# Performance work log

Hardware: AMD Instinct MI355X
Metric: run time of the kernel (lower is better)

Reference implementation:

```python
import jax, jax.numpy as jnp
import numpy as np

B, S, D = 2, 2048, 1024
H, HD = 16, 64  # num heads, head dim
EPS = 1e-12
SCALING = HD ** -0.5


def rotate_half(x):
    x1, x2 = jnp.split(x, 2, axis=-1)
    return jnp.concatenate([-x2, x1], axis=-1)


def setup_inputs() -> dict:
    key = jax.random.key(0)
    ks = jax.random.split(key, 12)
    hidden_states = jax.random.normal(ks[0], (B, S, D), dtype=jnp.float32)
    # RoPE tables (standard rotate-half convention)
    inv_freq = 1.0 / (10000.0 ** (np.arange(0, HD, 2, dtype=np.float32) / HD))
    pos = np.arange(S, dtype=np.float32)
    freqs = np.outer(pos, inv_freq)  # [S, HD/2]
    emb = np.concatenate([freqs, freqs], axis=-1)  # [S, HD]
    cos = jnp.asarray(np.cos(emb))
    sin = jnp.asarray(np.sin(emb))
    w = 0.02
    return {
        "hidden_states": hidden_states,
        "cos": cos,
        "sin": sin,
        "Wq": jax.random.normal(ks[1], (D, D), dtype=jnp.float32) * w,
        "bq": jnp.zeros((D,), dtype=jnp.float32),
        "Wk": jax.random.normal(ks[2], (D, D), dtype=jnp.float32) * w,
        "bk": jnp.zeros((D,), dtype=jnp.float32),
        "Wv": jax.random.normal(ks[3], (D, D), dtype=jnp.float32) * w,
        "bv": jnp.zeros((D,), dtype=jnp.float32),
        "Wo": jax.random.normal(ks[4], (D, D), dtype=jnp.float32) * w,
        "bo": jnp.zeros((D,), dtype=jnp.float32),
        "ln_w": jnp.ones((D,), dtype=jnp.float32),
        "ln_b": jnp.zeros((D,), dtype=jnp.float32),
    }


def reference(hidden_states, cos, sin, Wq, bq, Wk, bk, Wv, bv, Wo, bo, ln_w, ln_b):
    b, s, d = hidden_states.shape
    # QKV projections -> [b, h, s, hd]
    def proj(W, bias):
        return (hidden_states @ W.T + bias).reshape(b, s, H, HD).transpose(0, 2, 1, 3)
    q, k, v = proj(Wq, bq), proj(Wk, bk), proj(Wv, bv)
    # RoPE (cos/sin broadcast over batch and head dims)
    c = cos[None, None, :, :]
    sn = sin[None, None, :, :]
    q = q * c + rotate_half(q) * sn
    k = k * c + rotate_half(k) * sn
    # Faithful to source: query pre-scaled AND scaling applied inside attention
    q = q * SCALING
    scores = jnp.einsum("bhsd,bhtd->bhst", q, k) * SCALING
    attn = jax.nn.softmax(scores, axis=-1)
    ctx = jnp.einsum("bhst,bhtd->bhsd", attn, v)  # [b,h,s,hd]
    ctx = ctx.transpose(0, 2, 1, 3).reshape(b, s, d)
    # output dense + residual + LayerNorm
    out = ctx @ Wo.T + bo + hidden_states
    mu = jnp.mean(out, axis=-1, keepdims=True)
    var = jnp.var(out, axis=-1, keepdims=True)
    return (out - mu) / jnp.sqrt(var + EPS) * ln_w + ln_b
```

## Files before the change

### kernel.cpp

```cpp
#include <hip/hip_runtime.h>
#include <hip/hip_bf16.h>
#include <stdint.h>


typedef unsigned short ushort_t;
typedef short bf16x8 __attribute__((ext_vector_type(8)));
typedef float f32x4 __attribute__((ext_vector_type(4)));
typedef float f32x16 __attribute__((ext_vector_type(16)));
typedef unsigned short ushort8 __attribute__((ext_vector_type(8)));

#define LOG2E 1.4426950408889634f

__device__ __forceinline__ ushort_t f2b(float f) {
  uint32_t x = __builtin_bit_cast(uint32_t, f);
  return (ushort_t)((x + 0x7FFFu + ((x >> 16) & 1u)) >> 16);
}

__device__ __forceinline__ uint32_t cvt_pk_bf16(float lo, float hi) {
  uint32_t r;
  asm("v_cvt_pk_bf16_f32 %0, %1, %2" : "=v"(r) : "v"(lo), "v"(hi));
  return r;
}

__device__ __forceinline__ void permswap(uint32_t& a, uint32_t& b) {
  asm volatile("v_permlane32_swap_b32 %0, %1" : "+v"(a), "+v"(b));
}

__device__ __forceinline__ void gload16(const void* gptr, void* ldsptr) {
  __builtin_amdgcn_global_load_lds(
      (const __attribute__((address_space(1))) uint32_t*)gptr,
      (__attribute__((address_space(3))) uint32_t*)ldsptr, 16, 0, 0);
}

__global__ void cast_kernel(const float* __restrict__ src, ushort_t* __restrict__ dst, int n) {
  int i = (blockIdx.x * 256 + threadIdx.x) * 8;
  if (i >= n) return;
  const float4* s = (const float4*)(src + i);
  float4 a = s[0], b = s[1];
  ushort8 o = { f2b(a.x), f2b(a.y), f2b(a.z), f2b(a.w),
                f2b(b.x), f2b(b.y), f2b(b.z), f2b(b.w) };
  *(ushort8*)(dst + i) = o;
}

__global__ void cast4_kernel(const float* __restrict__ a, const float* __restrict__ b,
                             const float* __restrict__ c, const float* __restrict__ d2,
                             ushort_t* __restrict__ oa, ushort_t* __restrict__ ob,
                             ushort_t* __restrict__ oc, ushort_t* __restrict__ od) {
  const int which = blockIdx.x >> 9;
  const float* src = which == 0 ? a : which == 1 ? b : which == 2 ? c : d2;
  ushort_t* dst = which == 0 ? oa : which == 1 ? ob : which == 2 ? oc : od;
  int i = ((blockIdx.x & 511) * 256 + threadIdx.x) * 8;
  const float4* s = (const float4*)(src + i);
  float4 x = s[0], y = s[1];
  ushort8 o = { f2b(x.x), f2b(x.y), f2b(x.z), f2b(x.w),
                f2b(y.x), f2b(y.y), f2b(y.z), f2b(y.w) };
  *(ushort8*)(dst + i) = o;
}

__global__ __launch_bounds__(256) void gemm_qkv(
    const ushort_t* __restrict__ hid, const ushort_t* __restrict__ wq,
    const ushort_t* __restrict__ wk, const ushort_t* __restrict__ wv,
    const float* __restrict__ bq, const float* __restrict__ bk,
    const float* __restrict__ bv, const float* __restrict__ cosT,
    const float* __restrict__ sinT, ushort_t* __restrict__ qout,
    ushort_t* __restrict__ kout, ushort_t* __restrict__ vtout)
{
  constexpr int K = 1024;
  __shared__ uint4 SB[3072];
  const int which = blockIdx.z;
  const ushort_t* A;
  const ushort_t* Bm;
  const float* bias;
  int m0, n0;
  if (which == 0)      { A = hid; Bm = wq; bias = bq; m0 = blockIdx.x * 128; n0 = blockIdx.y * 128; }
  else if (which == 1) { A = hid; Bm = wk; bias = bk; m0 = blockIdx.x * 128; n0 = blockIdx.y * 128; }
  else                 { A = wv;  Bm = hid; bias = bv; m0 = blockIdx.y * 128; n0 = blockIdx.x * 128; }

  const int tid = threadIdx.x;
  const int wave = tid >> 6, lane = tid & 63;
  const int d = lane & 15, g = lane >> 4;
  const int wm = (wave >> 1) * 64, wn = (wave & 1) * 64;

  const ushort_t* ag = A + (size_t)(m0 + (tid >> 2)) * K + (tid & 3) * 8;
  const ushort_t* bg = Bm + (size_t)(n0 + (tid >> 2)) * K + (tid & 3) * 8;

  f32x4 acc[4][4] = {};

#define STAGE_Q(buf, k0)                                           \
  {                                                                \
    char* dst = (char*)SB + (buf) * 16384 + wave * 1024;           \
    gload16(ag + (k0), dst);                                       \
    gload16(ag + 64 * K + (k0), dst + 4096);                       \
    gload16(bg + (k0), dst + 8192);                                \
    gload16(bg + 64 * K + (k0), dst + 12288);                      \
  }

#define COMPUTE_Q(buf)                                                          \
  {                                                                             \
    bf16x8 af[4], bfr[4];                                                       \
    _Pragma("unroll") for (int i = 0; i < 4; ++i)                               \
        af[i] = __builtin_bit_cast(bf16x8,                                      \
            SB[(buf) * 1024 + (wm + i * 16 + d) * 4 + g]);                      \
    _Pragma("unroll") for (int j = 0; j < 4; ++j)                               \
        bfr[j] = __builtin_bit_cast(bf16x8,                                     \
            SB[(buf) * 1024 + 512 + (wn + j * 16 + d) * 4 + g]);                \
    _Pragma("unroll") for (int i = 0; i < 4; ++i)                               \
        _Pragma("unroll") for (int j = 0; j < 4; ++j)                           \
            acc[i][j] = __builtin_amdgcn_mfma_f32_16x16x32_bf16(                \
                af[i], bfr[j], acc[i][j], 0, 0, 0);                             \
  }

  STAGE_Q(0, 0);
  STAGE_Q(1, 32);
  asm volatile("s_waitcnt vmcnt(4)" ::: "memory");
  __builtin_amdgcn_s_barrier();

  int bufc = 0;
  for (int t = 0; t < 30; ++t) {
    int bufn = bufc + 2; if (bufn >= 3) bufn -= 3;
    STAGE_Q(bufn, (t + 2) * 32);
    COMPUTE_Q(bufc);
    asm volatile("s_waitcnt vmcnt(4)" ::: "memory");
    __builtin_amdgcn_s_barrier();
    bufc = (bufc == 2) ? 0 : bufc + 1;
  }
  COMPUTE_Q(bufc);
  asm volatile("s_waitcnt vmcnt(0)" ::: "memory");
  __builtin_amdgcn_s_barrier();
  bufc = (bufc == 2) ? 0 : bufc + 1;
  COMPUTE_Q(bufc);
#undef STAGE_Q
#undef COMPUTE_Q

  if (which <= 1) {
    ushort_t* O = which == 0 ? qout : kout;
    const float qscale = which == 0 ? (LOG2E / 64.0f) : 1.0f;
    const int head_base = n0 + wn;
    const int h = head_base >> 6;
#pragma unroll
    for (int i = 0; i < 4; ++i) {
#pragma unroll
      for (int r = 0; r < 4; ++r) {
        const int m = m0 + wm + i * 16 + g * 4 + r;
        const int s = m & 2047, b = m >> 11;
#pragma unroll
        for (int j = 0; j < 4; ++j) {
          const int c = j * 16 + d;
          const float v0 = acc[i][j][r] + bias[head_base + c];
          const float v1 = acc[i][j ^ 2][r] + bias[head_base + (c ^ 32)];
          const float rot = (c < 32) ? -v1 : v1;
          const float vr = (v0 * cosT[s * 64 + c] + rot * sinT[s * 64 + c]) * qscale;
          O[(size_t)(((b << 4) + h) * 2048 + s) * 64 + c] = f2b(vr);
        }
      }
    }
  } else {
    ushort_t* O = vtout;
#pragma unroll
    for (int i = 0; i < 4; ++i) {
#pragma unroll
      for (int r = 0; r < 4; ++r) {
        const int fr = m0 + wm + i * 16 + g * 4 + r;
        const float bv2 = bias[fr];
        const int h = fr >> 6, dd = fr & 63;
#pragma unroll
        for (int j = 0; j < 4; ++j) {
          const int tok = n0 + wn + j * 16 + d;
          const int b = tok >> 11, s = tok & 2047;
          O[(size_t)(((b << 4) + h) * 64 + dd) * 2048 + s] = f2b(acc[i][j][r] + bv2);
        }
      }
    }
  }
}

__global__ __launch_bounds__(256) void gemm_wo(
    const ushort_t* __restrict__ A, const ushort_t* __restrict__ B,
    const float* __restrict__ bias, const float* __restrict__ resid,
    float* __restrict__ O)
{
  constexpr int K = 1024;
  __shared__ uint4 SB[3072];
  const int tid = threadIdx.x;
  const int wave = tid >> 6, lane = tid & 63;
  const int d = lane & 15, g = lane >> 4;
  const int m0 = blockIdx.x * 128, n0 = blockIdx.y * 128;
  const int wm = (wave >> 1) * 64, wn = (wave & 1) * 64;

  const ushort_t* ag = A + (size_t)(m0 + (tid >> 2)) * K + (tid & 3) * 8;
  const ushort_t* bg = B + (size_t)(n0 + (tid >> 2)) * K + (tid & 3) * 8;

  f32x4 acc[4][4] = {};

#define STAGE_W(buf, k0)                                           \
  {                                                                \
    char* dst = (char*)SB + (buf) * 16384 + wave * 1024;           \
    gload16(ag + (k0), dst);                                       \
    gload16(ag + 64 * K + (k0), dst + 4096);                       \
    gload16(bg + (k0), dst + 8192);                                \
    gload16(bg + 64 * K + (k0), dst + 12288);                      \
  }

#define COMPUTE_W(buf)                                                          \
  {                                                                             \
    bf16x8 af[4], bfr[4];                                                       \
    _Pragma("unroll") for (int i = 0; i < 4; ++i)                               \
        af[i] = __builtin_bit_cast(bf16x8,                                      \
            SB[(buf) * 1024 + (wm + i * 16 + d) * 4 + g]);                      \
    _Pragma("unroll") for (int j = 0; j < 4; ++j)                               \
        bfr[j] = __builtin_bit_cast(bf16x8,                                     \
            SB[(buf) * 1024 + 512 + (wn + j * 16 + d) * 4 + g]);                \
    _Pragma("unroll") for (int i = 0; i < 4; ++i)                               \
        _Pragma("unroll") for (int j = 0; j < 4; ++j)                           \
            acc[i][j] = __builtin_amdgcn_mfma_f32_16x16x32_bf16(                \
                af[i], bfr[j], acc[i][j], 0, 0, 0);                             \
  }

  STAGE_W(0, 0);
  STAGE_W(1, 32);
  asm volatile("s_waitcnt vmcnt(4)" ::: "memory");
  __builtin_amdgcn_s_barrier();

  int bufc = 0;
  for (int t = 0; t < 30; ++t) {
    int bufn = bufc + 2; if (bufn >= 3) bufn -= 3;
    STAGE_W(bufn, (t + 2) * 32);
    COMPUTE_W(bufc);
    asm volatile("s_waitcnt vmcnt(4)" ::: "memory");
    __builtin_amdgcn_s_barrier();
    bufc = (bufc == 2) ? 0 : bufc + 1;
  }
  COMPUTE_W(bufc);
  asm volatile("s_waitcnt vmcnt(0)" ::: "memory");
  __builtin_amdgcn_s_barrier();
  bufc = (bufc == 2) ? 0 : bufc + 1;
  COMPUTE_W(bufc);
#undef STAGE_W
#undef COMPUTE_W

#pragma unroll
  for (int i = 0; i < 4; ++i)
#pragma unroll
    for (int r = 0; r < 4; ++r) {
      const int m = m0 + wm + i * 16 + g * 4 + r;
#pragma unroll
      for (int j = 0; j < 4; ++j) {
        const int n = n0 + wn + j * 16 + d;
        O[(size_t)m * 1024 + n] = acc[i][j][r] + bias[n] + resid[(size_t)m * 1024 + n];
      }
    }
}

__global__ __launch_bounds__(512) void attn_kernel(
    const ushort_t* __restrict__ Q, const ushort_t* __restrict__ Kb,
    const ushort_t* __restrict__ VT, ushort_t* __restrict__ ctx)
{
  __shared__ uint4 KV[2048];
  __shared__ float Ls[256];
  const int orig = blockIdx.x;
  const int wgid = (orig & 7) * 64 + (orig >> 3);
  const int bh = wgid >> 4;
  const int q0 = (wgid & 15) * 128;
  const int tid = threadIdx.x;
  const int wave = tid >> 6, lane = tid & 63;
  const int qw = wave >> 1, half = wave & 1;
  const int ql = lane & 31, h2 = lane >> 5;
  const int qrow = q0 + qw * 32 + ql;

  bf16x8 qf[4];
  {
    const ushort_t* qp = Q + ((size_t)bh * 2048 + qrow) * 64 + h2 * 8;
#pragma unroll
    for (int s = 0; s < 4; ++s)
      qf[s] = __builtin_bit_cast(bf16x8, *(const uint4*)(qp + 16 * s));
  }

  const int st_row = tid >> 3, st_c8 = tid & 7;
  const ushort_t* kgp = Kb + (size_t)(bh * 2048 + st_row) * 64 + st_c8 * 8;
  const ushort_t* vgp = VT + (size_t)(bh * 64 + st_row) * 2048 + st_c8 * 8;
  const int sidx = st_row * 8 + (st_c8 ^ (st_row & 7));

  uint4 kr = *(const uint4*)(kgp);
  uint4 vr = *(const uint4*)(vgp);
  KV[sidx] = kr;
  KV[512 + sidx] = vr;
  __syncthreads();

  float lsum = 0.f;
  f32x16 cacc[2] = {};

  for (int t = 0; t < 32; ++t) {
    const int cb = (t & 1) << 10;
    const int nb = ((t + 1) & 1) << 10;
    const int kvn = (t + 1) * 64;
    if (t < 31) {
      kr = *(const uint4*)(kgp + kvn * 64);
      vr = *(const uint4*)(vgp + kvn);
    }

    f32x16 z = {};
#pragma unroll
    for (int s = 0; s < 4; ++s) {
      bf16x8 kf = __builtin_bit_cast(bf16x8,
          KV[cb + (half * 32 + ql) * 8 + ((2 * s + h2) ^ (ql & 7))]);
      z = __builtin_amdgcn_mfma_f32_32x32x16_bf16(kf, qf[s], z, 0, 0, 0);
    }

    bf16x8 pf[2];
#pragma unroll
    for (int s2 = 0; s2 < 2; ++s2) {
      const int rb = s2 * 8;
      float p0 = __builtin_amdgcn_exp2f(z[rb + 0]);
      float p1 = __builtin_amdgcn_exp2f(z[rb + 1]);
      float p2 = __builtin_amdgcn_exp2f(z[rb + 2]);
      float p3 = __builtin_amdgcn_exp2f(z[rb + 3]);
      float p4 = __builtin_amdgcn_exp2f(z[rb + 4]);
      float p5 = __builtin_amdgcn_exp2f(z[rb + 5]);
      float p6 = __builtin_amdgcn_exp2f(z[rb + 6]);
      float p7 = __builtin_amdgcn_exp2f(z[rb + 7]);
      lsum += ((p0 + p1) + (p2 + p3)) + ((p4 + p5) + (p6 + p7));
      uint32_t a1 = cvt_pk_bf16(p0, p1);
      uint32_t a2 = cvt_pk_bf16(p2, p3);
      uint32_t b1 = cvt_pk_bf16(p4, p5);
      uint32_t b2 = cvt_pk_bf16(p6, p7);
      permswap(a1, b1);
      permswap(a2, b2);
      uint4 u = {a1, a2, b1, b2};
      pf[s2] = __builtin_bit_cast(bf16x8, u);
    }

#pragma unroll
    for (int dt = 0; dt < 2; ++dt)
#pragma unroll
      for (int s2 = 0; s2 < 2; ++s2) {
        const int s = 2 * half + s2;
        bf16x8 vf = __builtin_bit_cast(bf16x8,
            KV[cb + 512 + (dt * 32 + ql) * 8 + ((2 * s + h2) ^ (ql & 7))]);
        cacc[dt] = __builtin_amdgcn_mfma_f32_32x32x16_bf16(vf, pf[s2], cacc[dt], 0, 0, 0);
      }

    if (t < 31) {
      KV[nb + sidx] = kr;
      KV[nb + 512 + sidx] = vr;
    }
    __syncthreads();
  }

  float* Lf = (float*)KV;
  const int slot = qw * 64 + lane;
  if (half == 1) {
#pragma unroll
    for (int dt = 0; dt < 2; ++dt)
#pragma unroll
      for (int r = 0; r < 16; ++r)
        Lf[slot * 32 + ((dt * 16 + r) ^ (lane & 31))] = cacc[dt][r];
    Ls[slot] = lsum;
  }
  __syncthreads();
  if (half == 0) {
#pragma unroll
    for (int dt = 0; dt < 2; ++dt)
#pragma unroll
      for (int r = 0; r < 16; ++r)
        cacc[dt][r] += Lf[slot * 32 + ((dt * 16 + r) ^ (lane & 31))];
    lsum += Ls[slot];

    lsum += __shfl_xor(lsum, 32, 64);
    const float rinv = 1.0f / lsum;
    const int b = bh >> 4, h = bh & 15;
    ushort_t* cp = ctx + ((size_t)(b * 2048 + qrow)) * 1024 + h * 64 + h2 * 4;
#pragma unroll
    for (int dt = 0; dt < 2; ++dt)
#pragma unroll
      for (int t = 0; t < 4; ++t) {
        uint2 w;
        w.x = cvt_pk_bf16(cacc[dt][4 * t + 0] * rinv, cacc[dt][4 * t + 1] * rinv);
        w.y = cvt_pk_bf16(cacc[dt][4 * t + 2] * rinv, cacc[dt][4 * t + 3] * rinv);
        *(uint2*)(cp + dt * 32 + t * 8) = w;
      }
  }
}

__global__ __launch_bounds__(256) void ln_kernel(const float* __restrict__ x,
    const float* __restrict__ w, const float* __restrict__ b2, float* __restrict__ out)
{
  const int row = blockIdx.x, tid = threadIdx.x;
  const float4 v = ((const float4*)(x + (size_t)row * 1024))[tid];
  float s = v.x + v.y + v.z + v.w;
  float ss = v.x * v.x + v.y * v.y + v.z * v.z + v.w * v.w;
#pragma unroll
  for (int off = 32; off > 0; off >>= 1) {
    s += __shfl_down(s, off, 64);
    ss += __shfl_down(ss, off, 64);
  }
  __shared__ float red[8];
  if ((tid & 63) == 0) { red[tid >> 6] = s; red[4 + (tid >> 6)] = ss; }
  __syncthreads();
  const float S = red[0] + red[1] + red[2] + red[3];
  const float SS = red[4] + red[5] + red[6] + red[7];
  const float mu = S * (1.f / 1024.f);
  const float rstd = rsqrtf(SS * (1.f / 1024.f) - mu * mu + 1e-12f);
  const int c = tid * 4;
  float4 o;
  o.x = (v.x - mu) * rstd * w[c + 0] + b2[c + 0];
  o.y = (v.y - mu) * rstd * w[c + 1] + b2[c + 1];
  o.z = (v.z - mu) * rstd * w[c + 2] + b2[c + 2];
  o.w = (v.w - mu) * rstd * w[c + 3] + b2[c + 3];
  ((float4*)(out + (size_t)row * 1024))[tid] = o;
}

extern "C" void kernel_launch(void* const* d_in, const int* in_sizes, int n_in,
                              void* d_out, int out_size, void* d_ws, size_t ws_size,
                              hipStream_t stream) {
  const float* hidden = (const float*)d_in[0];
  const float* cosT = (const float*)d_in[1];
  const float* sinT = (const float*)d_in[2];
  const float* Wq = (const float*)d_in[3];
  const float* bq = (const float*)d_in[4];
  const float* Wk = (const float*)d_in[5];
  const float* bk = (const float*)d_in[6];
  const float* Wv = (const float*)d_in[7];
  const float* bv = (const float*)d_in[8];
  const float* Wo = (const float*)d_in[9];
  const float* bo = (const float*)d_in[10];
  const float* lnw = (const float*)d_in[11];
  const float* lnb = (const float*)d_in[12];

  char* ws = (char*)d_ws;
  const size_t MB = 1u << 20;
  ushort_t* hid_bf = (ushort_t*)(ws);
  ushort_t* wq_bf = (ushort_t*)(ws + 8 * MB);
  ushort_t* wk_bf = (ushort_t*)(ws + 10 * MB);
  ushort_t* wv_bf = (ushort_t*)(ws + 12 * MB);
  ushort_t* wo_bf = (ushort_t*)(ws + 14 * MB);
  ushort_t* q_buf = (ushort_t*)(ws + 16 * MB);
  ushort_t* k_buf = (ushort_t*)(ws + 24 * MB);
  ushort_t* vt_buf = (ushort_t*)(ws + 32 * MB);
  ushort_t* ctx_bf = (ushort_t*)(ws + 40 * MB);
  float* out_pre = (float*)(ws + 16 * MB);

  cast_kernel<<<2048, 256, 0, stream>>>(hidden, hid_bf, 4194304);
  cast4_kernel<<<2048, 256, 0, stream>>>(Wq, Wk, Wv, Wo, wq_bf, wk_bf, wv_bf, wo_bf);

  gemm_qkv<<<dim3(32, 8, 3), 256, 0, stream>>>(hid_bf, wq_bf, wk_bf, wv_bf,
                                               bq, bk, bv, cosT, sinT,
                                               q_buf, k_buf, vt_buf);
  attn_kernel<<<512, 512, 0, stream>>>(q_buf, k_buf, vt_buf, ctx_bf);
  gemm_wo<<<dim3(32, 8), 256, 0, stream>>>(ctx_bf, wo_bf, bo, hidden, out_pre);
  ln_kernel<<<4096, 256, 0, stream>>>(out_pre, lnw, lnb, (float*)d_out);
}
```

Measured before the change: 111.8 us.

## Merge cast kernels, compute softmax row sums via MFMA, unroll attention loop by two

Merges the hidden-state and weight bf16 cast kernels into one launch, saving a kernel launch. In attention, the scalar exp-sum accumulation and the final cross-lane shuffle are replaced by an extra MFMA that multiplies the probabilities by a ones vector. This moves the row-sum additions onto the matrix unit, at the cost of two extra MFMAs per tile. The KV double-buffer loop is manually unrolled by two with fixed buffer offsets, removing per-iteration index arithmetic and one barrier on the final step.

Result: faster. 109.4 us (-2.1%).

```diff
diff --git a/kernel.cpp b/kernel.cpp
--- a/kernel.cpp
+++ b/kernel.cpp
@@ -32,24 +32,24 @@
       (__attribute__((address_space(3))) uint32_t*)ldsptr, 16, 0, 0);
 }
 
-__global__ void cast_kernel(const float* __restrict__ src, ushort_t* __restrict__ dst, int n) {
-  int i = (blockIdx.x * 256 + threadIdx.x) * 8;
-  if (i >= n) return;
-  const float4* s = (const float4*)(src + i);
-  float4 a = s[0], b = s[1];
-  ushort8 o = { f2b(a.x), f2b(a.y), f2b(a.z), f2b(a.w),
-                f2b(b.x), f2b(b.y), f2b(b.z), f2b(b.w) };
-  *(ushort8*)(dst + i) = o;
-}
-
-__global__ void cast4_kernel(const float* __restrict__ a, const float* __restrict__ b,
-                             const float* __restrict__ c, const float* __restrict__ d2,
-                             ushort_t* __restrict__ oa, ushort_t* __restrict__ ob,
-                             ushort_t* __restrict__ oc, ushort_t* __restrict__ od) {
-  const int which = blockIdx.x >> 9;
-  const float* src = which == 0 ? a : which == 1 ? b : which == 2 ? c : d2;
-  ushort_t* dst = which == 0 ? oa : which == 1 ? ob : which == 2 ? oc : od;
-  int i = ((blockIdx.x & 511) * 256 + threadIdx.x) * 8;
+__global__ void cast_all_kernel(const float* __restrict__ h,
+                                const float* __restrict__ a, const float* __restrict__ b,
+                                const float* __restrict__ c, const float* __restrict__ d2,
+                                ushort_t* __restrict__ oh, ushort_t* __restrict__ oa,
+                                ushort_t* __restrict__ ob, ushort_t* __restrict__ oc,
+                                ushort_t* __restrict__ od) {
+  const int blk = blockIdx.x;
+  const float* src;
+  ushort_t* dst;
+  int rel;
+  if (blk < 2048) { src = h; dst = oh; rel = blk; }
+  else {
+    const int w = (blk - 2048) >> 9;
+    rel = (blk - 2048) & 511;
+    src = w == 0 ? a : w == 1 ? b : w == 2 ? c : d2;
+    dst = w == 0 ? oa : w == 1 ? ob : w == 2 ? oc : od;
+  }
+  const int i = (rel * 256 + threadIdx.x) * 8;
   const float4* s = (const float4*)(src + i);
   float4 x = s[0], y = s[1];
   ushort8 o = { f2b(x.x), f2b(x.y), f2b(x.z), f2b(x.w),
@@ -275,6 +275,12 @@
       qf[s] = __builtin_bit_cast(bf16x8, *(const uint4*)(qp + 16 * s));
   }
 
+  bf16x8 onesf;
+  {
+    uint4 ou = {0x3F803F80u, 0x3F803F80u, 0x3F803F80u, 0x3F803F80u};
+    onesf = __builtin_bit_cast(bf16x8, ou);
+  }
+
   const int st_row = tid >> 3, st_c8 = tid & 7;
   const ushort_t* kgp = Kb + (size_t)(bh * 2048 + st_row) * 64 + st_c8 * 8;
   const ushort_t* vgp = VT + (size_t)(bh * 64 + st_row) * 2048 + st_c8 * 8;
@@ -286,66 +292,77 @@
   KV[512 + sidx] = vr;
   __syncthreads();
 
-  float lsum = 0.f;
   f32x16 cacc[2] = {};
-
-  for (int t = 0; t < 32; ++t) {
-    const int cb = (t & 1) << 10;
-    const int nb = ((t + 1) & 1) << 10;
-    const int kvn = (t + 1) * 64;
-    if (t < 31) {
-      kr = *(const uint4*)(kgp + kvn * 64);
-      vr = *(const uint4*)(vgp + kvn);
+  f32x16 lacc = {};
+
+#define ATT_COMPUTE(CB)                                                         \
+  {                                                                             \
+    f32x16 z = {};                                                              \
+    _Pragma("unroll") for (int s = 0; s < 4; ++s) {                             \
+      bf16x8 kf = __builtin_bit_cast(bf16x8,                                    \
+          KV[(CB) + (half * 32 + ql) * 8 + ((2 * s + h2) ^ (ql & 7))]);         \
+      z = __builtin_amdgcn_mfma_f32_32x32x16_bf16(kf, qf[s], z, 0, 0, 0);       \
+    }                                                                           \
+    bf16x8 pf[2];                                                               \
+    _Pragma("unroll") for (int s2 = 0; s2 < 2; ++s2) {                          \
+      const int rb = s2 * 8;                                                    \
+      float p0 = __builtin_amdgcn_exp2f(z[rb + 0]);                             \
+      float p1 = __builtin_amdgcn_exp2f(z[rb + 1]);                             \
+      float p2 = __builtin_amdgcn_exp2f(z[rb + 2]);                             \
+      float p3 = __builtin_amdgcn_exp2f(z[rb + 3]);                             \
+      float p4 = __builtin_amdgcn_exp2f(z[rb + 4]);                             \
+      float p5 = __builtin_amdgcn_exp2f(z[rb + 5]);                             \
+      float p6 = __builtin_amdgcn_exp2f(z[rb + 6]);                             \
+      float p7 = __builtin_amdgcn_exp2f(z[rb + 7]);                             \
+      uint32_t a1 = cvt_pk_bf16(p0, p1);                                        \
+      uint32_t a2 = cvt_pk_bf16(p2, p3);                                        \
+      uint32_t b1 = cvt_pk_bf16(p4, p5);                                        \
+      uint32_t b2 = cvt_pk_bf16(p6, p7);                                        \
+      permswap(a1, b1);                                                         \
+      permswap(a2, b2);                                                         \
+      uint4 u = {a1, a2, b1, b2};                                               \
+      pf[s2] = __builtin_bit_cast(bf16x8, u);                                   \
+    }                                                                           \
+    _Pragma("unroll") for (int s2 = 0; s2 < 2; ++s2)                            \
+      lacc = __builtin_amdgcn_mfma_f32_32x32x16_bf16(onesf, pf[s2], lacc,       \
+                                                     0, 0, 0);                  \
+    _Pragma("unroll") for (int dt = 0; dt < 2; ++dt)                            \
+      _Pragma("unroll") for (int s2 = 0; s2 < 2; ++s2) {                        \
+        const int s = 2 * half + s2;                                            \
+        bf16x8 vf = __builtin_bit_cast(bf16x8,                                  \
+            KV[(CB) + 512 + (dt * 32 + ql) * 8 + ((2 * s + h2) ^ (ql & 7))]);   \
+        cacc[dt] = __builtin_amdgcn_mfma_f32_32x32x16_bf16(vf, pf[s2],          \
+                                                           cacc[dt], 0, 0, 0); \
+      }                                                                         \
+  }
+
+  const ushort_t* kP = kgp + 4096;
+  const ushort_t* vP = vgp + 64;
+  for (int tt = 0; tt < 16; ++tt) {
+    kr = *(const uint4*)(kP);
+    vr = *(const uint4*)(vP);
+    ATT_COMPUTE(0)
+    KV[1024 + sidx] = kr;
+    KV[1536 + sidx] = vr;
+    __syncthreads();
+    if (tt < 15) {
+      kr = *(const uint4*)(kP + 4096);
+      vr = *(const uint4*)(vP + 64);
     }
-
-    f32x16 z = {};
-#pragma unroll
-    for (int s = 0; s < 4; ++s) {
-      bf16x8 kf = __builtin_bit_cast(bf16x8,
-          KV[cb + (half * 32 + ql) * 8 + ((2 * s + h2) ^ (ql & 7))]);
-      z = __builtin_amdgcn_mfma_f32_32x32x16_bf16(kf, qf[s], z, 0, 0, 0);
+    ATT_COMPUTE(1024)
+    if (tt < 15) {
+      KV[sidx] = kr;
+      KV[512 + sidx] = vr;
+      __syncthreads();
     }
-
-    bf16x8 pf[2];
-#pragma unroll
-    for (int s2 = 0; s2 < 2; ++s2) {
-      const int rb = s2 * 8;
-      float p0 = __builtin_amdgcn_exp2f(z[rb + 0]);
-      float p1 = __builtin_amdgcn_exp2f(z[rb + 1]);
-      float p2 = __builtin_amdgcn_exp2f(z[rb + 2]);
-      float p3 = __builtin_amdgcn_exp2f(z[rb + 3]);
-      float p4 = __builtin_amdgcn_exp2f(z[rb + 4]);
-      float p5 = __builtin_amdgcn_exp2f(z[rb + 5]);
-      float p6 = __builtin_amdgcn_exp2f(z[rb + 6]);
-      float p7 = __builtin_amdgcn_exp2f(z[rb + 7]);
-      lsum += ((p0 + p1) + (p2 + p3)) + ((p4 + p5) + (p6 + p7));
-      uint32_t a1 = cvt_pk_bf16(p0, p1);
-      uint32_t a2 = cvt_pk_bf16(p2, p3);
-      uint32_t b1 = cvt_pk_bf16(p4, p5);
-      uint32_t b2 = cvt_pk_bf16(p6, p7);
-      permswap(a1, b1);
-      permswap(a2, b2);
-      uint4 u = {a1, a2, b1, b2};
-      pf[s2] = __builtin_bit_cast(bf16x8, u);
-    }
-
-#pragma unroll
-    for (int dt = 0; dt < 2; ++dt)
-#pragma unroll
-      for (int s2 = 0; s2 < 2; ++s2) {
-        const int s = 2 * half + s2;
-        bf16x8 vf = __builtin_bit_cast(bf16x8,
-            KV[cb + 512 + (dt * 32 + ql) * 8 + ((2 * s + h2) ^ (ql & 7))]);
-        cacc[dt] = __builtin_amdgcn_mfma_f32_32x32x16_bf16(vf, pf[s2], cacc[dt], 0, 0, 0);
-      }
-
-    if (t < 31) {
-      KV[nb + sidx] = kr;
-      KV[nb + 512 + sidx] = vr;
-    }
-    __syncthreads();
-  }
-
+    kP += 8192;
+    vP += 128;
+  }
+#undef ATT_COMPUTE
+
+  float lsum = lacc[0];
+
+  __syncthreads();
   float* Lf = (float*)KV;
   const int slot = qw * 64 + lane;
   if (half == 1) {
@@ -365,7 +382,6 @@
         cacc[dt][r] += Lf[slot * 32 + ((dt * 16 + r) ^ (lane & 31))];
     lsum += Ls[slot];
 
-    lsum += __shfl_xor(lsum, 32, 64);
     const float rinv = 1.0f / lsum;
     const int b = bh >> 4, h = bh & 15;
     ushort_t* cp = ctx + ((size_t)(b * 2048 + qrow)) * 1024 + h * 64 + h2 * 4;
@@ -439,8 +455,8 @@
   ushort_t* ctx_bf = (ushort_t*)(ws + 40 * MB);
   float* out_pre = (float*)(ws + 16 * MB);
 
-  cast_kernel<<<2048, 256, 0, stream>>>(hidden, hid_bf, 4194304);
-  cast4_kernel<<<2048, 256, 0, stream>>>(Wq, Wk, Wv, Wo, wq_bf, wk_bf, wv_bf, wo_bf);
+  cast_all_kernel<<<4096, 256, 0, stream>>>(hidden, Wq, Wk, Wv, Wo,
+                                            hid_bf, wq_bf, wk_bf, wv_bf, wo_bf);
 
   gemm_qkv<<<dim3(32, 8, 3), 256, 0, stream>>>(hid_bf, wq_bf, wk_bf, wv_bf,
                                                bq, bk, bv, cosT, sinT,
```
